# Optimization experiments

Hardware: AMD Instinct MI355X
Metric: run time of the kernel (lower is better)

Reference implementation:

```python
import jax, jax.numpy as jnp
import numpy as np

B, T, N, D, W = 8, 24, 1024, 64, 2
EPS = 1e-5


def setup_inputs() -> dict:
    key = jax.random.key(0)
    ks = jax.random.split(key, 6)
    s = 1.0 / np.sqrt(D)
    x = jax.random.normal(ks[0], (B, T, N, D), dtype=jnp.float32)
    W1 = jax.random.normal(ks[1], (D, D), dtype=jnp.float32) * s
    b1 = jax.random.normal(ks[2], (D,), dtype=jnp.float32) * s
    W2 = jax.random.normal(ks[3], (D, D), dtype=jnp.float32) * s
    b2 = jax.random.normal(ks[4], (D,), dtype=jnp.float32) * s
    gamma = jnp.ones((D,), dtype=jnp.float32)
    beta = jnp.zeros((D,), dtype=jnp.float32)
    # expanded_adj: [N, N*W] = [I | I | ...], then row-normalized (norm_adj ~ D^-1 A)
    adj = jnp.tile(jnp.eye(N, dtype=jnp.float32), (1, W))
    adj = adj / jnp.clip(adj.sum(axis=1, keepdims=True), 1.0, None)
    return {"x": x, "W1": W1, "b1": b1, "W2": W2, "b2": b2,
            "gamma": gamma, "beta": beta, "adj": adj}


def reference(x, W1, b1, W2, b2, gamma, beta, adj):
    Bx, Tx, Nx, Dx = x.shape
    win = adj.shape[1] // Nx
    feat = jnp.pad(x, ((0, 0), (win - 1, 0), (0, 0), (0, 0)))
    g = jnp.stack([feat[:, i:i + Tx] for i in range(win)], axis=2)
    g = g.reshape(Bx, Tx, win * Nx, Dx)
    h1 = jnp.einsum('btmd,ed->btme', g, W1) + b1
    h2 = jnp.einsum('btmd,ed->btme', g, W2) + b2
    a1 = jnp.einsum('nm,btme->btne', adj, h1)  # [B,T,N,D]
    a2 = jnp.einsum('nm,btme->btne', adj, h2)
    full = jax.nn.relu(a1 * a2) + a1
    z = full + x
    mu = z.mean(axis=-1, keepdims=True)
    var = z.var(axis=-1, keepdims=True)
    return (z - mu) * jax.lax.rsqrt(var + EPS) * gamma + beta
```

## Files before the change

### kernel.cpp

```cpp
#include <hip/hip_runtime.h>

#define BB 8
#define TT 24
#define NN 1024
#define DD 64
#define WW 2

typedef float  f32x4  __attribute__((ext_vector_type(4)));
typedef __bf16 bf16x8 __attribute__((ext_vector_type(8)));

#define LOADC(dst, ptr) do {                         \
    dst[0] = *(const f32x4*)((ptr) + q8);            \
    dst[1] = *(const f32x4*)((ptr) + q8 + 4);        \
    dst[2] = *(const f32x4*)((ptr) + 32 + q8);       \
    dst[3] = *(const f32x4*)((ptr) + 36 + q8);       \
} while (0)

#define STEP(K, PRV, CUR, DO_PREF, C0K) do {                                       \
    const size_t off = off0 + (size_t)(K) * (NN * DD);                             \
    const float* xr = x + off;                                                     \
        \
    bf16x8 X0, X1;                                                                 \
    _Pragma("unroll")                                                              \
    for (int j = 0; j < 4; ++j) {                                                  \
        X0[j]     = (__bf16)((C0K) * PRV[0][j] + c1 * CUR[0][j]);                  \
        X0[j + 4] = (__bf16)((C0K) * PRV[1][j] + c1 * CUR[1][j]);                  \
        X1[j]     = (__bf16)((C0K) * PRV[2][j] + c1 * CUR[2][j]);                  \
        X1[j + 4] = (__bf16)((C0K) * PRV[3][j] + c1 * CUR[3][j]);                  \
    }                                                                              \
                   \
    if (DO_PREF) { LOADC(PRV, xr + NN * DD); }                                     \
      \
    f32x4 xe[4];                                                                   \
    _Pragma("unroll")                                                              \
    for (int et = 0; et < 4; ++et)                                                 \
        xe[et] = *(const f32x4*)(xr + et * 16 + e4);                               \
                        \
    f32x4 acc1[4], acc2[4];                                                        \
    _Pragma("unroll")                                                              \
    for (int et = 0; et < 4; ++et) {                                               \
        acc1[et] = (f32x4){0.f, 0.f, 0.f, 0.f};                                    \
        acc2[et] = (f32x4){0.f, 0.f, 0.f, 0.f};                                    \
    }                                                                              \
    _Pragma("unroll")                                                              \
    for (int et = 0; et < 4; ++et) {                                               \
        const bf16x8 w10 = wlds[et * 2 + 0][lane];                                 \
        const bf16x8 w11 = wlds[et * 2 + 1][lane];                                 \
        const bf16x8 w20 = wlds[8 + et * 2 + 0][lane];                             \
        const bf16x8 w21 = wlds[8 + et * 2 + 1][lane];                             \
        acc1[et] = __builtin_amdgcn_mfma_f32_16x16x32_bf16(w10, X0, acc1[et], 0, 0, 0); \
        acc1[et] = __builtin_amdgcn_mfma_f32_16x16x32_bf16(w11, X1, acc1[et], 0, 0, 0); \
        acc2[et] = __builtin_amdgcn_mfma_f32_16x16x32_bf16(w20, X0, acc2[et], 0, 0, 0); \
        acc2[et] = __builtin_amdgcn_mfma_f32_16x16x32_bf16(w21, X1, acc2[et], 0, 0, 0); \
    }                                                                              \
             \
    float s = 0.f, s2 = 0.f;                                                       \
    _Pragma("unroll")                                                              \
    for (int et = 0; et < 4; ++et) {                                               \
        const f32x4 b1v = *(const f32x4*)(b1 + et * 16 + e4);                      \
        const f32x4 b2v = *(const f32x4*)(b2 + et * 16 + e4);                      \
        _Pragma("unroll")                                                          \
        for (int r = 0; r < 4; ++r) {                                              \
            const float A1v = acc1[et][r] + cb * b1v[r];                           \
            const float A2v = acc2[et][r] + cb * b2v[r];                           \
            const float p   = A1v * A2v;                                           \
            const float full = (p > 0.f ? p : 0.f) + A1v;                          \
            const float zz = full + xe[et][r];                                     \
            acc1[et][r] = zz;                                                      \
            s  += zz;                                                              \
            s2 += zz * zz;                                                         \
        }                                                                          \
    }                                                                              \
    s  += __shfl_xor(s, 16, 64);                                                   \
    s2 += __shfl_xor(s2, 16, 64);                                                  \
    s  += __shfl_xor(s, 32, 64);                                                   \
    s2 += __shfl_xor(s2, 32, 64);                                                  \
    const float mu  = s * (1.f / 64.f);                                            \
    const float var = s2 * (1.f / 64.f) - mu * mu;                                 \
    const float rs  = rsqrtf(var + 1e-5f);                                         \
    float* orow = out + off;                                                       \
    _Pragma("unroll")                                                              \
    for (int et = 0; et < 4; ++et) {                                               \
        const f32x4 gvv = *(const f32x4*)(gamma + et * 16 + e4);                   \
        const f32x4 bev = *(const f32x4*)(beta  + et * 16 + e4);                   \
        f32x4 o;                                                                   \
        _Pragma("unroll")                                                          \
        for (int r = 0; r < 4; ++r)                                                \
            o[r] = (acc1[et][r] - mu) * rs * gvv[r] + bev[r];                      \
        *(f32x4*)(orow + et * 16 + e4) = o;                                        \
    }                                                                              \
} while (0)

__global__ __launch_bounds__(256) void stgcn_kernel(
    const float* __restrict__ x,
    const float* __restrict__ W1,
    const float* __restrict__ b1,
    const float* __restrict__ W2,
    const float* __restrict__ b2,
    const float* __restrict__ gamma,
    const float* __restrict__ beta,
    const float* __restrict__ adj,
    float* __restrict__ out)
{
    const int lane = threadIdx.x & 63;
    const int wv   = threadIdx.x >> 6;
    const int m16  = lane & 15;
    const int quad = lane >> 4;
    const int e4   = quad * 4;
    const int q8   = quad * 8;

    __shared__ bf16x8 wlds[16][64];
    for (int s = threadIdx.x; s < 16 * 64; s += 256) {
        const int g  = s >> 6, l = s & 63;
        const int mat = g >> 3, et = (g >> 1) & 3, ks = g & 1;
        const int ms = l & 15, qs = l >> 4;
        const float* src = (mat ? W2 : W1) + (et * 16 + ms) * DD + ks * 32 + qs * 8;
        const f32x4 a = *(const f32x4*)(src);
        const f32x4 b = *(const f32x4*)(src + 4);
        bf16x8 f;
#pragma unroll
        for (int j = 0; j < 4; ++j) { f[j] = (__bf16)a[j]; f[j + 4] = (__bf16)b[j]; }
        wlds[g][l] = f;
    }
    __syncthreads();

    const int wid = blockIdx.x * 4 + wv;
    const int nt  = wid & 63;
    const int tg  = (wid >> 6) & 7;
    const int b   = wid >> 9;
    const int t0  = tg * 3;

    const int n = nt * 16 + m16;
    const float c0 = adj[(size_t)n * (NN * WW) + n];
    const float c1 = adj[(size_t)n * (NN * WW) + NN + n];
    const float cb = c0 + c1;

    const size_t off0 = ((size_t)(b * TT + t0) * NN + nt * 16 + m16) * DD;

    f32x4 bufA[4], bufB[4];
    LOADC(bufB, x + off0);
    if (t0 > 0) {
        LOADC(bufA, x + off0 - NN * DD);
    } else {
        bufA[0] = bufA[1] = bufA[2] = bufA[3] = (f32x4){0.f, 0.f, 0.f, 0.f};
    }
    const float c00 = (t0 > 0) ? c0 : 0.f;

    STEP(0, bufA, bufB, 1, c00);
    STEP(1, bufB, bufA, 1, c0);
    STEP(2, bufA, bufB, 0, c0);
}

extern "C" void kernel_launch(void* const* d_in, const int* in_sizes, int n_in,
                              void* d_out, int out_size, void* d_ws, size_t ws_size,
                              hipStream_t stream) {
    const float* x     = (const float*)d_in[0];
    const float* W1    = (const float*)d_in[1];
    const float* b1    = (const float*)d_in[2];
    const float* W2    = (const float*)d_in[3];
    const float* b2    = (const float*)d_in[4];
    const float* gamma = (const float*)d_in[5];
    const float* beta  = (const float*)d_in[6];
    const float* adj   = (const float*)d_in[7];
    float* out = (float*)d_out;

    dim3 grid(1024), block(256);
    hipLaunchKernelGGL(stgcn_kernel, grid, block, 0, stream,
                       x, W1, b1, W2, b2, gamma, beta, adj, out);
}
```

Before: 128.5 us.

## Lengthen per-wave time chain to four, stage params in LDS, reorder loads

```diff
diff --git a/kernel.cpp b/kernel.cpp
--- a/kernel.cpp
+++ b/kernel.cpp
@@ -4,7 +4,7 @@
 #define TT 24
 #define NN 1024
 #define DD 64
-#define WW 2
+#define CHAIN 4
 
 typedef float  f32x4  __attribute__((ext_vector_type(4)));
 typedef __bf16 bf16x8 __attribute__((ext_vector_type(8)));
@@ -19,7 +19,12 @@
 #define STEP(K, PRV, CUR, DO_PREF, C0K) do {                                       \
     const size_t off = off0 + (size_t)(K) * (NN * DD);                             \
     const float* xr = x + off;                                                     \
-        \
+            \
+    f32x4 xe[4];                                                                   \
+    _Pragma("unroll")                                                              \
+    for (int et = 0; et < 4; ++et)                                                 \
+        xe[et] = *(const f32x4*)(xr + et * 16 + e4);                               \
+          \
     bf16x8 X0, X1;                                                                 \
     _Pragma("unroll")                                                              \
     for (int j = 0; j < 4; ++j) {                                                  \
@@ -28,13 +33,10 @@
         X1[j]     = (__bf16)((C0K) * PRV[2][j] + c1 * CUR[2][j]);                  \
         X1[j + 4] = (__bf16)((C0K) * PRV[3][j] + c1 * CUR[3][j]);                  \
     }                                                                              \
-                   \
+          \
+    __builtin_amdgcn_sched_barrier(0);                                             \
+                 \
     if (DO_PREF) { LOADC(PRV, xr + NN * DD); }                                     \
-      \
-    f32x4 xe[4];                                                                   \
-    _Pragma("unroll")                                                              \
-    for (int et = 0; et < 4; ++et)                                                 \
-        xe[et] = *(const f32x4*)(xr + et * 16 + e4);                               \
                         \
     f32x4 acc1[4], acc2[4];                                                        \
     _Pragma("unroll")                                                              \
@@ -53,12 +55,12 @@
         acc2[et] = __builtin_amdgcn_mfma_f32_16x16x32_bf16(w20, X0, acc2[et], 0, 0, 0); \
         acc2[et] = __builtin_amdgcn_mfma_f32_16x16x32_bf16(w21, X1, acc2[et], 0, 0, 0); \
     }                                                                              \
-             \
+       \
     float s = 0.f, s2 = 0.f;                                                       \
     _Pragma("unroll")                                                              \
     for (int et = 0; et < 4; ++et) {                                               \
-        const f32x4 b1v = *(const f32x4*)(b1 + et * 16 + e4);                      \
-        const f32x4 b2v = *(const f32x4*)(b2 + et * 16 + e4);                      \
+        const f32x4 b1v = plds[0][et * 4 + quad];                                  \
+        const f32x4 b2v = plds[1][et * 4 + quad];                                  \
         _Pragma("unroll")                                                          \
         for (int r = 0; r < 4; ++r) {                                              \
             const float A1v = acc1[et][r] + cb * b1v[r];                           \
@@ -81,8 +83,8 @@
     float* orow = out + off;                                                       \
     _Pragma("unroll")                                                              \
     for (int et = 0; et < 4; ++et) {                                               \
-        const f32x4 gvv = *(const f32x4*)(gamma + et * 16 + e4);                   \
-        const f32x4 bev = *(const f32x4*)(beta  + et * 16 + e4);                   \
+        const f32x4 gvv = plds[2][et * 4 + quad];                                  \
+        const f32x4 bev = plds[3][et * 4 + quad];                                  \
         f32x4 o;                                                                   \
         _Pragma("unroll")                                                          \
         for (int r = 0; r < 4; ++r)                                                \
@@ -102,38 +104,47 @@
     const float* __restrict__ adj,
     float* __restrict__ out)
 {
-    const int lane = threadIdx.x & 63;
-    const int wv   = threadIdx.x >> 6;
+    const int tid  = threadIdx.x;
+    const int lane = tid & 63;
+    const int wv   = tid >> 6;
     const int m16  = lane & 15;
     const int quad = lane >> 4;
     const int e4   = quad * 4;
     const int q8   = quad * 8;
 
     __shared__ bf16x8 wlds[16][64];
-    for (int s = threadIdx.x; s < 16 * 64; s += 256) {
+    __shared__ f32x4  plds[4][16];
+
+    for (int s = tid; s < 16 * 64; s += 256) {
         const int g  = s >> 6, l = s & 63;
         const int mat = g >> 3, et = (g >> 1) & 3, ks = g & 1;
         const int ms = l & 15, qs = l >> 4;
         const float* src = (mat ? W2 : W1) + (et * 16 + ms) * DD + ks * 32 + qs * 8;
-        const f32x4 a = *(const f32x4*)(src);
-        const f32x4 b = *(const f32x4*)(src + 4);
+        const f32x4 a  = *(const f32x4*)(src);
+        const f32x4 bb = *(const f32x4*)(src + 4);
         bf16x8 f;
 #pragma unroll
-        for (int j = 0; j < 4; ++j) { f[j] = (__bf16)a[j]; f[j + 4] = (__bf16)b[j]; }
+        for (int j = 0; j < 4; ++j) { f[j] = (__bf16)a[j]; f[j + 4] = (__bf16)bb[j]; }
         wlds[g][l] = f;
+    }
+    if (tid < 64) {
+        const int arr = tid >> 4, j = tid & 15;
+        const float* src = (arr == 0) ? b1 : (arr == 1) ? b2 : (arr == 2) ? gamma : beta;
+        plds[arr][j] = *(const f32x4*)(src + j * 4);
     }
     __syncthreads();
 
     const int wid = blockIdx.x * 4 + wv;
     const int nt  = wid & 63;
-    const int tg  = (wid >> 6) & 7;
-    const int b   = wid >> 9;
-    const int t0  = tg * 3;
+    const int tg  = (wid >> 6) % 6;
+    const int b   = wid / 384;
+    const int t0  = tg * CHAIN;
 
     const int n = nt * 16 + m16;
-    const float c0 = adj[(size_t)n * (NN * WW) + n];
-    const float c1 = adj[(size_t)n * (NN * WW) + NN + n];
+    const float c0 = adj[(size_t)n * (NN * 2) + n];
+    const float c1 = adj[(size_t)n * (NN * 2) + NN + n];
     const float cb = c0 + c1;
+    const float c00 = (t0 > 0) ? c0 : 0.f;
 
     const size_t off0 = ((size_t)(b * TT + t0) * NN + nt * 16 + m16) * DD;
 
@@ -144,11 +155,11 @@
     } else {
         bufA[0] = bufA[1] = bufA[2] = bufA[3] = (f32x4){0.f, 0.f, 0.f, 0.f};
     }
-    const float c00 = (t0 > 0) ? c0 : 0.f;
 
     STEP(0, bufA, bufB, 1, c00);
     STEP(1, bufB, bufA, 1, c0);
-    STEP(2, bufA, bufB, 0, c0);
+    STEP(2, bufA, bufB, 1, c0);
+    STEP(3, bufB, bufA, 0, c0);
 }
 
 extern "C" void kernel_launch(void* const* d_in, const int* in_sizes, int n_in,
@@ -164,7 +175,7 @@
     const float* adj   = (const float*)d_in[7];
     float* out = (float*)d_out;
 
-    dim3 grid(1024), block(256);
+    dim3 grid(768), block(256);
     hipLaunchKernelGGL(stgcn_kernel, grid, block, 0, stream,
                        x, W1, b1, W2, b2, gamma, beta, adj, out);
 }
```

New measurement: 123.7 us. 3.8% less time.
